# Performance work log

Hardware: AMD Instinct MI355X
Metric: run time of the kernel (lower is better)

## Reference

```python
import jax, jax.numpy as jnp
import numpy as np

P = 20            # corr_patch_size: displacement offsets in [-10, 9]
B, C, H, W = 8, 64, 64, 192


def _leaky(x):
    return jax.nn.leaky_relu(x, 0.1)


def _conv3d(x, w, b, stride, pad, groups):
    y = jax.lax.conv_general_dilated(
        x, w, window_strides=(stride, stride, stride),
        padding=[(pad, pad)] * 3,
        dimension_numbers=('NCDHW', 'OIDHW', 'NCDHW'),
        feature_group_count=groups)
    return y + b[None, :, None, None, None]


def _block(x, dw_w, dw_b, pw_w, pw_b, stride):
    # depthwise 3x3x3 (strided) -> LeakyReLU -> pointwise 1x1x1 -> LeakyReLU
    x = _leaky(_conv3d(x, dw_w, dw_b, stride, 1, x.shape[1]))
    x = _leaky(_conv3d(x, pw_w, pw_b, 1, 0, 1))
    return x


def _correlation(rgb, depth):
    # SpatialCorrelationSampler(kernel_size=1, patch_size=P, stride=1):
    # corr[b, di, dj, y, x] = sum_c rgb[b,c,y,x] * depth[b,c, y+di-P//2, x+dj-P//2]
    pad_lo, pad_hi = P // 2, P - 1 - P // 2   # offsets -10 .. 9
    dp = jnp.pad(depth, ((0, 0), (0, 0), (pad_lo, pad_hi), (pad_lo, pad_hi)))
    rows = []
    for di in range(P):                       # structural loop over patch rows
        dh = dp[:, :, di:di + H, :]           # [B, C, H, W+P-1]
        # all P horizontal shifts at once: [B, P, C, H, W]
        win = jnp.stack([dh[:, :, :, dj:dj + W] for dj in range(P)], axis=1)
        rows.append(jnp.einsum('bchw,bpchw->bphw', rgb, win))
    return jnp.stack(rows, axis=1)            # [B, P, P, H, W]


def setup_inputs() -> dict:
    key = jax.random.key(0)
    ks = jax.random.split(key, 12)

    def rn(k, shape, scale=0.05):
        return jax.random.normal(k, shape, jnp.float32) * scale

    return {
        'rgb_branch': jax.random.normal(ks[0], (B, C, H, W), jnp.float32),
        'depth_branch': jax.random.normal(ks[1], (B, C, H, W), jnp.float32),
        'dw1_w': rn(ks[2], (20, 1, 3, 3, 3)), 'dw1_b': jnp.zeros((20,), jnp.float32),
        'pw1_w': rn(ks[3], (20, 20, 1, 1, 1)), 'pw1_b': jnp.zeros((20,), jnp.float32),
        'dw2_w': rn(ks[4], (20, 1, 3, 3, 3)), 'dw2_b': jnp.zeros((20,), jnp.float32),
        'pw2_w': rn(ks[5], (40, 20, 1, 1, 1)), 'pw2_b': jnp.zeros((40,), jnp.float32),
        'dw3_w': rn(ks[6], (40, 1, 3, 3, 3)), 'dw3_b': jnp.zeros((40,), jnp.float32),
        'pw3_w': rn(ks[7], (40, 40, 1, 1, 1)), 'pw3_b': jnp.zeros((40,), jnp.float32),
        'dw4_w': rn(ks[8], (40, 1, 3, 3, 3)), 'dw4_b': jnp.zeros((40,), jnp.float32),
        'pw4_w': rn(ks[9], (80, 40, 1, 1, 1)), 'pw4_b': jnp.zeros((80,), jnp.float32),
    }


def reference(rgb_branch, depth_branch,
              dw1_w, dw1_b, pw1_w, pw1_b,
              dw2_w, dw2_b, pw2_w, pw2_b,
              dw3_w, dw3_b, pw3_w, pw3_b,
              dw4_w, dw4_b, pw4_w, pw4_b):
    corr = _correlation(rgb_branch, depth_branch)          # [B,20,20,H,W]
    out = _block(corr, dw1_w, dw1_b, pw1_w, pw1_b, 1)      # [B,20,20,H,W]
    out = _block(out, dw2_w, dw2_b, pw2_w, pw2_b, 2)       # [B,40,10,H/2,W/2]
    out = _block(out, dw3_w, dw3_b, pw3_w, pw3_b, 1)
    out = _block(out, dw4_w, dw4_b, pw4_w, pw4_b, 2)       # [B,80,5,H/4,W/4]
    return out
```

## Files before the change

### kernel.cpp

```cpp
#include <hip/hip_runtime.h>
#include <cstdint>
#include <cstddef>


typedef unsigned short u16;
typedef _Float16 f16_t;
typedef __attribute__((ext_vector_type(2))) _Float16 half2_t;
typedef __attribute__((ext_vector_type(8))) _Float16 half8_t;
typedef __attribute__((ext_vector_type(4))) float f32x4;

static __device__ inline u16 f2h(float f) {
    union { f16_t h; u16 u; } v; v.h = (f16_t)f; return v.u;
}
static __device__ inline half2_t H2(uint32_t u) {
    union { uint32_t u; half2_t h; } v; v.u = u; return v.h;
}

#if __has_builtin(__builtin_amdgcn_fdot2)
static __device__ inline float FDOT2(half2_t a, half2_t b, float c) {
    return __builtin_amdgcn_fdot2(a, b, c, false);
}
#else
static __device__ inline float FDOT2(half2_t a, half2_t b, float c) {
    return fmaf((float)a.x, (float)b.x, fmaf((float)a.y, (float)b.y, c));
}
#endif

#if __has_builtin(__builtin_amdgcn_alignbit)
static __device__ inline uint32_t mkp(uint32_t lo, uint32_t hi) {
    return __builtin_amdgcn_alignbit(hi, lo, 16);
}
#else
static __device__ inline uint32_t mkp(uint32_t lo, uint32_t hi) {
    return (lo >> 16) | (hi << 16);
}
#endif

static __device__ inline uint32_t ldu(const u16* p) { return *(const uint32_t*)p; }

__global__ __launch_bounds__(256) void transpose_f16(
        const float* __restrict__ rgb, const float* __restrict__ dep,
        u16* __restrict__ rgbT, u16* __restrict__ depT) {
    const int bh = blockIdx.x;
    const float* src = blockIdx.y ? dep : rgb;
    u16* dst = blockIdx.y ? depT : rgbT;
    const int tid = threadIdx.x;
    const int b = bh >> 6, h = bh & 63;

    __shared__ u16 S[64 * 194];

    const float* srcb = src + (size_t)b * 786432 + (size_t)h * 192;
#pragma unroll
    for (int it = 0; it < 12; ++it) {
        const int idx = it * 256 + tid;
        const int c = idx / 48, w4 = idx - c * 48;
        const float4 v = *(const float4*)(srcb + (size_t)c * 12288 + 4 * w4);
        u16* sp = &S[c * 194 + 4 * w4];
        sp[0] = f2h(v.x); sp[1] = f2h(v.y); sp[2] = f2h(v.z); sp[3] = f2h(v.w);
    }
    __syncthreads();
    u16* dstb = dst + (size_t)bh * 192 * 64;
#pragma unroll
    for (int it = 0; it < 12; ++it) {
        const int idx = it * 256 + tid;
        const int w = idx >> 4, c4 = idx & 15;
        ushort4 o;
        o.x = S[(4 * c4 + 0) * 194 + w];
        o.y = S[(4 * c4 + 1) * 194 + w];
        o.z = S[(4 * c4 + 2) * 194 + w];
        o.w = S[(4 * c4 + 3) * 194 + w];
        *(ushort4*)(dstb + (size_t)w * 64 + 4 * c4) = o;
    }
}

__global__ __launch_bounds__(256) void corr_mfma(
        const u16* __restrict__ rgbT, const u16* __restrict__ depT,
        u16* __restrict__ out) {
    const int idx = blockIdx.x;
    const int band = idx & 7;
    const int j    = idx >> 3;
    const int dig  = j % 5;
    const int rest = j / 5;
    const int h    = band * 8 + (rest & 7);
    const int b    = rest >> 3;
    const int tid = threadIdx.x;
    const int lane = tid & 63, wave = tid >> 6;
    const int n = lane & 15, q = lane >> 4;
    const int w0base = wave * 48;

    __shared__ u16 D4[4][4080];

    const u16* Abase = rgbT + (size_t)(b * 64 + h) * 12288;
    half8_t a0[3], a1[3];
#pragma unroll
    for (int t = 0; t < 3; ++t) {
        const half8_t* Ap = (const half8_t*)(Abase + (size_t)(w0base + t * 16 + n) * 64 + q * 8);
        a0[t] = Ap[0];
        a1[t] = Ap[4];
    }

#pragma unroll
    for (int i = 0; i < 4; ++i) {
        const int di = dig * 4 + i;
        const int hd = h + di - 10;
        if (hd < 0 || hd >= 64) continue;

        const u16* Bbase = depT + (size_t)(b * 64 + hd) * 12288;
        half8_t B0[5], B1[5];
#pragma unroll
        for (int k = 0; k < 5; ++k) {
            const int u0 = w0base + (k - 1) * 16;
            if (u0 >= 0 && u0 <= 176) {
                const half8_t* Bp = (const half8_t*)(Bbase + (size_t)(u0 + n) * 64 + q * 8);
                B0[k] = Bp[0];
                B1[k] = Bp[4];
            } else {
                B0[k] = (half8_t)(f16_t)0.f;
                B1[k] = (half8_t)(f16_t)0.f;
            }
        }
#pragma unroll
        for (int t = 0; t < 3; ++t) {
            const int w0 = w0base + t * 16;
            f32x4 acc[3];
#pragma unroll
            for (int ut = 0; ut < 3; ++ut) {
                acc[ut].x = 0.f; acc[ut].y = 0.f; acc[ut].z = 0.f; acc[ut].w = 0.f;
            }
#pragma unroll
            for (int ut = 0; ut < 3; ++ut) {
                const int k = t + ut;
                acc[ut] = __builtin_amdgcn_mfma_f32_16x16x32_f16(a0[t], B0[k], acc[ut], 0, 0, 0);
                acc[ut] = __builtin_amdgcn_mfma_f32_16x16x32_f16(a1[t], B1[k], acc[ut], 0, 0, 0);
            }
#pragma unroll
            for (int ut = 0; ut < 3; ++ut) {
#pragma unroll
                for (int r = 0; r < 4; ++r) {
                    const int dj = 16 * ut + n - 4 * q - r - 6;
                    const int w = w0 + 4 * q + r;
                    if (dj >= 0 && dj < 20)
                        D4[i][w * 21 + (w >> 2) + dj] = f2h(acc[ut][r]);
                }
            }
        }
    }

#pragma unroll
    for (int i = 0; i < 4; ++i) {
        const int di = dig * 4 + i;
        const int hd = h + di - 10;
        const bool valid = (hd >= 0) && (hd < 64);
        u16* outb = out + ((size_t)((b * 20 + di) * 20) * 64 + h) * 192;
#pragma unroll
        for (int it = 0; it < 4; ++it) {
            const int item = it * 64 + lane;
            if (item < 240) {
                const int dj = item / 12;
                const int w4 = wave * 12 + (item - dj * 12);
                ushort4 o;
                if (valid) {
                    const int base = 85 * w4 + dj;
                    o.x = D4[i][base];
                    o.y = D4[i][base + 21];
                    o.z = D4[i][base + 42];
                    o.w = D4[i][base + 63];
                } else {
                    o = make_ushort4(0, 0, 0, 0);
                }
                *(ushort4*)(outb + (size_t)dj * 12288 + 4 * w4) = o;
            }
        }
    }
}

template<int CIN, int COUT, int S, int DT, int DIN, int HIN, int WIN,
         int DO, int HO, int WO, typename TOUT>
static __device__ __forceinline__ void fused_impl(
        const u16* __restrict__ x,
        const float* __restrict__ dw_w, const float* __restrict__ dw_b,
        const float* __restrict__ pw_w, const float* __restrict__ pw_b,
        TOUT* __restrict__ y) {
    static_assert(WO % 48 == 0 && HO % 4 == 0, "tile divisibility");
    constexpr int CINP = (CIN == 20) ? 22 : 42;
    constexpr int NTASK = CIN * 12;
    constexpr int WT = WO / 48;
    constexpr int NP = S * (DT - 1) + 3;
    constexpr int ROWS = 3 * S + 3;
    constexpr int NL = (S == 1) ? 4 : 5;
    constexpr int G  = (S == 1) ? 6 : 3;
    constexpr int NG = ROWS / G;

    const int wt = blockIdx.x % WT;
    const int ht = blockIdx.x / WT;
    const int d0 = blockIdx.y * DT;
    const int b  = blockIdx.z;
    const int tid = threadIdx.x;
    const int h0 = ht * 4;
    const int wbase = wt * 48;

    __shared__ float sDW[CIN * 27];
    __shared__ float sDB[CIN];
    __shared__ u16   sT[DT * 4 * 48 * CINP + 16];

    for (int i = tid; i < CIN * 27; i += 256) sDW[i] = dw_w[i];
    for (int i = tid; i < CIN; i += 256) sDB[i] = dw_b[i];
    __syncthreads();

    for (int idx = tid; idx < NTASK; idx += 256) {
        const int ci = idx / 12;
        const int wg = idx - ci * 12;
        const int w0g = wbase + wg * 4;
        const int offA = (w0g > 0) ? -2 : 0;

        half2_t KA[9], KB[9];
#pragma unroll
        for (int t = 0; t < 9; ++t) {
            const int kd = t / 3, kh = t - 3 * kd;
            const float k0 = sDW[ci * 27 + kd * 9 + kh * 3 + 0];
            const float k1 = sDW[ci * 27 + kd * 9 + kh * 3 + 1];
            const float k2 = sDW[ci * 27 + kd * 9 + kh * 3 + 2];
            half2_t a; a.x = (f16_t)k0; a.y = (f16_t)k1; KA[t] = a;
            half2_t bb;
            if constexpr (S == 1) { bb.x = (f16_t)k2; bb.y = (f16_t)0.f; }
            else                  { bb.x = (f16_t)0.f; bb.y = (f16_t)k2; }
            KB[t] = bb;
        }

        float acc[DT][4][4];
#pragma unroll
        for (int dl = 0; dl < DT; ++dl)
#pragma unroll
            for (int a = 0; a < 4; ++a)
#pragma unroll
                for (int c = 0; c < 4; ++c) acc[dl][a][c] = 0.f;

        const u16* plane0 = x + (size_t)(b * CIN + ci) * DIN * HIN * WIN;
#pragma unroll
        for (int p = 0; p < NP; ++p) {
            const int din = S * d0 - 1 + p;
            if (din < 0 || din >= DIN) continue;
            const u16* pl = plane0 + (size_t)din * HIN * WIN;
#pragma unroll
            for (int g = 0; g < NG; ++g) {
                uint32_t R[G][NL];
#pragma unroll
                for (int rr = 0; rr < G; ++rr) {
                    const int r = g * G + rr;
                    int hin = h0 * S - 1 + r;
                    int hc = hin < 0 ? 0 : (hin >= HIN ? HIN - 1 : hin);
                    const u16* rowp = pl + (size_t)hc * WIN + (size_t)w0g * S;
                    R[rr][0] = ldu(rowp + offA);
                    R[rr][1] = ldu(rowp);
                    R[rr][2] = ldu(rowp + 2);
                    R[rr][3] = ldu(rowp + 4);
                    if constexpr (S == 2) R[rr][4] = ldu(rowp + 6);
                }
#pragma unroll
                for (int rr = 0; rr < G; ++rr) {
                    const int r = g * G + rr;
                    const int hin = h0 * S - 1 + r;
                    uint32_t D0 = R[rr][0], D1 = R[rr][1];
                    uint32_t D2 = R[rr][2], D3 = R[rr][3];
                    uint32_t E4 = 0;
                    if constexpr (S == 2) E4 = R[rr][4];
                    D0 = (w0g > 0) ? D0 : 0u;
                    if constexpr (S == 1) D3 = (w0g + 4 < WIN) ? D3 : 0u;
                    if constexpr (S == 1) {
                        if (r == 0 || r == ROWS - 1) {
                            const bool rv = (hin >= 0) && (hin < HIN);
                            if (!rv) { D0 = 0; D1 = 0; D2 = 0; D3 = 0; }
                        }
                    } else {
                        if (r == 0) {
                            const bool rv = (hin >= 0);
                            if (!rv) { D0 = 0; D1 = 0; D2 = 0; D3 = 0; E4 = 0; }
                        }
                    }
                    uint32_t PA[4], PB[4];
                    if constexpr (S == 1) {
                        const uint32_t m01 = mkp(D0, D1);
                        const uint32_t m12 = mkp(D1, D2);
                        const uint32_t m23 = mkp(D2, D3);
                        PA[0] = m01; PA[1] = D1; PA[2] = m12; PA[3] = D2;
                        PB[0] = m12; PB[1] = D2; PB[2] = m23; PB[3] = D3;
                    } else {
                        PA[0] = mkp(D0, D1); PA[1] = mkp(D1, D2);
                        PA[2] = mkp(D2, D3); PA[3] = mkp(D3, E4);
                        PB[0] = D1; PB[1] = D2; PB[2] = D3; PB[3] = E4;
                    }
#pragma unroll
                    for (int dl = 0; dl < DT; ++dl) {
                        const int kd = p - S * dl;
                        if (kd < 0 || kd > 2) continue;
#pragma unroll
                        for (int hh = 0; hh < 4; ++hh) {
                            const int kh = r - S * hh;
                            if (kh < 0 || kh > 2) continue;
                            const int t = kd * 3 + kh;
#pragma unroll
                            for (int k = 0; k < 4; ++k)
                                acc[dl][hh][k] = FDOT2(H2(PB[k]), KB[t],
                                                 FDOT2(H2(PA[k]), KA[t],
                                                       acc[dl][hh][k]));
                        }
                    }
                }
            }
        }

        const float bia = sDB[ci];
#pragma unroll
        for (int dl = 0; dl < DT; ++dl) {
#pragma unroll
            for (int hh = 0; hh < 4; ++hh) {
#pragma unroll
                for (int k = 0; k < 4; ++k) {
                    const float t = acc[dl][hh][k] + bia;
                    sT[((dl * 4 + hh) * 48 + wg * 4 + k) * CINP + ci] =
                        f2h(fmaxf(t, 0.1f * t));
                }
            }
        }
    }
    __syncthreads();

    constexpr int NT = (COUT + 15) / 16;
    constexpr int KH = (CIN + 31) / 32;
    constexpr int MTW = DT * 3;
    const int lane = tid & 63, wave = tid >> 6;
    const int m15 = lane & 15, q = lane >> 4;

    half8_t bf[NT][KH];
    float   pb[NT];
#pragma unroll
    for (int nt = 0; nt < NT; ++nt) {
        const int co = nt * 16 + m15;
        pb[nt] = (co < COUT) ? pw_b[co] : 0.f;
#pragma unroll
        for (int kh = 0; kh < KH; ++kh) {
            union { half8_t v; f16_t e[8]; } u;
#pragma unroll
            for (int j = 0; j < 8; ++j) {
                const int ci = kh * 32 + q * 8 + j;
                u.e[j] = (co < COUT && ci < CIN)
                         ? (f16_t)pw_w[co * CIN + ci] : (f16_t)0.f;
            }
            bf[nt][kh] = u.v;
        }
    }

    const size_t planeSz = (size_t)DO * HO * WO;
    for (int mt = wave * MTW; mt < (wave + 1) * MTW; ++mt) {
        const int dl  = mt / 12;
        const int rem = mt - dl * 12;
        const int hh  = rem / 3;
        const int w0  = (rem - hh * 3) * 16;
        if (d0 + dl >= DO) continue;

        const int pos0 = (dl * 4 + hh) * 48 + w0 + m15;
        const u16* ap = &sT[(size_t)pos0 * CINP];
        union { uint32_t u[4]; half8_t v; } af[KH];
#pragma unroll
        for (int kh = 0; kh < KH; ++kh) {
            const int ci0 = kh * 32 + q * 8;
            af[kh].u[0] = (ci0     < CIN) ? ldu(ap + ci0)     : 0u;
            af[kh].u[1] = (ci0 + 2 < CIN) ? ldu(ap + ci0 + 2) : 0u;
            af[kh].u[2] = (ci0 + 4 < CIN) ? ldu(ap + ci0 + 4) : 0u;
            af[kh].u[3] = (ci0 + 6 < CIN) ? ldu(ap + ci0 + 6) : 0u;
        }
#pragma unroll
        for (int nt = 0; nt < NT; ++nt) {
            f32x4 acc;
            acc.x = 0.f; acc.y = 0.f; acc.z = 0.f; acc.w = 0.f;
#pragma unroll
            for (int kh = 0; kh < KH; ++kh)
                acc = __builtin_amdgcn_mfma_f32_16x16x32_f16(
                          af[kh].v, bf[nt][kh], acc, 0, 0, 0);
            const int co = nt * 16 + m15;
            if (co < COUT) {
                const float bias = pb[nt];
                TOUT* yp = y + (size_t)b * COUT * planeSz + (size_t)co * planeSz
                             + (size_t)(d0 + dl) * HO * WO
                             + (size_t)(h0 + hh) * WO + wbase + w0 + q * 4;
                float s0 = acc.x + bias, s1 = acc.y + bias;
                float s2 = acc.z + bias, s3 = acc.w + bias;
                s0 = fmaxf(s0, 0.1f * s0); s1 = fmaxf(s1, 0.1f * s1);
                s2 = fmaxf(s2, 0.1f * s2); s3 = fmaxf(s3, 0.1f * s3);
                if constexpr (sizeof(TOUT) == 4) {
                    float4 o; o.x = s0; o.y = s1; o.z = s2; o.w = s3;
                    *(float4*)yp = o;
                } else {
                    ushort4 o;
                    o.x = f2h(s0); o.y = f2h(s1); o.z = f2h(s2); o.w = f2h(s3);
                    *(ushort4*)yp = o;
                }
            }
        }
    }
}

__global__ __launch_bounds__(256) void fb1_dwpw(
        const u16* __restrict__ x, const float* __restrict__ dww,
        const float* __restrict__ dwb, const float* __restrict__ pww,
        const float* __restrict__ pwb, u16* __restrict__ y) {
    fused_impl<20, 20, 1, 2, 20, 64, 192, 20, 64, 192, u16>(x, dww, dwb, pww, pwb, y);
}
__global__ __launch_bounds__(256) void fb2_dwpw(
        const u16* __restrict__ x, const float* __restrict__ dww,
        const float* __restrict__ dwb, const float* __restrict__ pww,
        const float* __restrict__ pwb, u16* __restrict__ y) {
    fused_impl<20, 40, 2, 2, 20, 64, 192, 10, 32, 96, u16>(x, dww, dwb, pww, pwb, y);
}
__global__ __launch_bounds__(256) void fb3_dwpw(
        const u16* __restrict__ x, const float* __restrict__ dww,
        const float* __restrict__ dwb, const float* __restrict__ pww,
        const float* __restrict__ pwb, u16* __restrict__ y) {
    fused_impl<40, 40, 1, 1, 10, 32, 96, 10, 32, 96, u16>(x, dww, dwb, pww, pwb, y);
}
__global__ __launch_bounds__(256) void fb4_dwpw(
        const u16* __restrict__ x, const float* __restrict__ dww,
        const float* __restrict__ dwb, const float* __restrict__ pww,
        const float* __restrict__ pwb, float* __restrict__ y) {
    fused_impl<40, 80, 2, 1, 10, 32, 96, 5, 16, 48, float>(x, dww, dwb, pww, pwb, y);
}

extern "C" void kernel_launch(void* const* d_in, const int* in_sizes, int n_in,
                              void* d_out, int out_size, void* d_ws, size_t ws_size,
                              hipStream_t stream) {
    const float* rgb  = (const float*)d_in[0];
    const float* dep  = (const float*)d_in[1];
    const float* dw1w = (const float*)d_in[2];
    const float* dw1b = (const float*)d_in[3];
    const float* pw1w = (const float*)d_in[4];
    const float* pw1b = (const float*)d_in[5];
    const float* dw2w = (const float*)d_in[6];
    const float* dw2b = (const float*)d_in[7];
    const float* pw2w = (const float*)d_in[8];
    const float* pw2b = (const float*)d_in[9];
    const float* dw3w = (const float*)d_in[10];
    const float* dw3b = (const float*)d_in[11];
    const float* pw3w = (const float*)d_in[12];
    const float* pw3b = (const float*)d_in[13];
    const float* dw4w = (const float*)d_in[14];
    const float* dw4b = (const float*)d_in[15];
    const float* pw4w = (const float*)d_in[16];
    const float* pw4b = (const float*)d_in[17];

    const size_t HALF = 78643200;
    u16* corrO = (u16*)d_ws;
    u16* rgbT  = (u16*)((char*)d_ws + HALF);
    u16* depT  = (u16*)((char*)d_ws + HALF + 12582912);
    u16* b1o   = (u16*)((char*)d_ws + HALF);
    u16* b2o   = (u16*)d_ws;
    u16* b3o   = (u16*)((char*)d_ws + HALF);
    float* outp = (float*)d_out;

    transpose_f16<<<dim3(512, 2), 256, 0, stream>>>(rgb, dep, rgbT, depT);

    corr_mfma<<<dim3(2560), 256, 0, stream>>>(rgbT, depT, corrO);

    fb1_dwpw<<<dim3(64, 10, 8), 256, 0, stream>>>(corrO, dw1w, dw1b, pw1w, pw1b, b1o);
    fb2_dwpw<<<dim3(16, 5, 8), 256, 0, stream>>>(b1o, dw2w, dw2b, pw2w, pw2b, b2o);
    fb3_dwpw<<<dim3(16, 10, 8), 256, 0, stream>>>(b2o, dw3w, dw3b, pw3w, pw3b, b3o);
    fb4_dwpw<<<dim3(4, 5, 8), 256, 0, stream>>>(b3o, dw4w, dw4b, pw4w, pw4b, outp);
}
```

Before: 353.1 us.

## Double-buffer depthwise input row loads and hoist pointwise weight gather

Restructures the depthwise loop into flattened batches over (depth plane, row group) and uses two register buffers, so the global loads for the next batch are issued before computing the current one. Out-of-range depth planes are now clamped and loaded, then skipped at compute time. Pointwise weight gathering moves before the first barrier when it is small, or into the gap before the second barrier otherwise, to overlap its global latency. All four kernels also get launch_bounds min-blocks of 4, which caps registers per thread and may cause spills given the larger live register set.

```diff
diff --git a/kernel.cpp b/kernel.cpp
--- a/kernel.cpp
+++ b/kernel.cpp
@@ -190,6 +190,9 @@
     constexpr int NL = (S == 1) ? 4 : 5;
     constexpr int G  = (S == 1) ? 6 : 3;
     constexpr int NG = ROWS / G;
+    constexpr int NB = NP * NG;
+    constexpr int NT = (COUT + 15) / 16;
+    constexpr int KH = (CIN + 31) / 32;
 
     const int wt = blockIdx.x % WT;
     const int ht = blockIdx.x / WT;
@@ -205,6 +208,31 @@
 
     for (int i = tid; i < CIN * 27; i += 256) sDW[i] = dw_w[i];
     for (int i = tid; i < CIN; i += 256) sDB[i] = dw_b[i];
+
+    const int lane = tid & 63, wave = tid >> 6;
+    const int m15 = lane & 15, q = lane >> 4;
+
+    half8_t bf[NT][KH];
+    float   pb[NT];
+    auto gather_w = [&]() {
+#pragma unroll
+        for (int nt = 0; nt < NT; ++nt) {
+            const int co = nt * 16 + m15;
+            pb[nt] = (co < COUT) ? pw_b[co] : 0.f;
+#pragma unroll
+            for (int kh = 0; kh < KH; ++kh) {
+                union { half8_t v; f16_t e[8]; } u;
+#pragma unroll
+                for (int jj = 0; jj < 8; ++jj) {
+                    const int ci = kh * 32 + q * 8 + jj;
+                    u.e[jj] = (co < COUT && ci < CIN)
+                              ? (f16_t)pw_w[co * CIN + ci] : (f16_t)0.f;
+                }
+                bf[nt][kh] = u.v;
+            }
+        }
+    };
+    if constexpr (NT * KH <= 4) gather_w();
     __syncthreads();
 
     for (int idx = tid; idx < NTASK; idx += 256) {
@@ -236,77 +264,91 @@
                 for (int c = 0; c < 4; ++c) acc[dl][a][c] = 0.f;
 
         const u16* plane0 = x + (size_t)(b * CIN + ci) * DIN * HIN * WIN;
-#pragma unroll
-        for (int p = 0; p < NP; ++p) {
+
+        uint32_t Rb[2][G * NL];
+
+        auto load_batch = [&](int bi, uint32_t* R) {
+            const int p = bi / NG;
+            const int g = bi - p * NG;
+            int din = S * d0 - 1 + p;
+            int dc = din < 0 ? 0 : (din >= DIN ? DIN - 1 : din);
+            const u16* pl = plane0 + (size_t)dc * HIN * WIN;
+#pragma unroll
+            for (int rr = 0; rr < G; ++rr) {
+                const int r = g * G + rr;
+                int hin = h0 * S - 1 + r;
+                int hc = hin < 0 ? 0 : (hin >= HIN ? HIN - 1 : hin);
+                const u16* rowp = pl + (size_t)hc * WIN + (size_t)w0g * S;
+                R[rr * NL + 0] = ldu(rowp + offA);
+                R[rr * NL + 1] = ldu(rowp);
+                R[rr * NL + 2] = ldu(rowp + 2);
+                R[rr * NL + 3] = ldu(rowp + 4);
+                if constexpr (S == 2) R[rr * NL + 4] = ldu(rowp + 6);
+            }
+        };
+
+        auto compute_batch = [&](int bi, const uint32_t* R) {
+            const int p = bi / NG;
+            const int g = bi - p * NG;
             const int din = S * d0 - 1 + p;
-            if (din < 0 || din >= DIN) continue;
-            const u16* pl = plane0 + (size_t)din * HIN * WIN;
-#pragma unroll
-            for (int g = 0; g < NG; ++g) {
-                uint32_t R[G][NL];
-#pragma unroll
-                for (int rr = 0; rr < G; ++rr) {
-                    const int r = g * G + rr;
-                    int hin = h0 * S - 1 + r;
-                    int hc = hin < 0 ? 0 : (hin >= HIN ? HIN - 1 : hin);
-                    const u16* rowp = pl + (size_t)hc * WIN + (size_t)w0g * S;
-                    R[rr][0] = ldu(rowp + offA);
-                    R[rr][1] = ldu(rowp);
-                    R[rr][2] = ldu(rowp + 2);
-                    R[rr][3] = ldu(rowp + 4);
-                    if constexpr (S == 2) R[rr][4] = ldu(rowp + 6);
-                }
-#pragma unroll
-                for (int rr = 0; rr < G; ++rr) {
-                    const int r = g * G + rr;
-                    const int hin = h0 * S - 1 + r;
-                    uint32_t D0 = R[rr][0], D1 = R[rr][1];
-                    uint32_t D2 = R[rr][2], D3 = R[rr][3];
-                    uint32_t E4 = 0;
-                    if constexpr (S == 2) E4 = R[rr][4];
-                    D0 = (w0g > 0) ? D0 : 0u;
-                    if constexpr (S == 1) D3 = (w0g + 4 < WIN) ? D3 : 0u;
-                    if constexpr (S == 1) {
-                        if (r == 0 || r == ROWS - 1) {
-                            const bool rv = (hin >= 0) && (hin < HIN);
-                            if (!rv) { D0 = 0; D1 = 0; D2 = 0; D3 = 0; }
-                        }
-                    } else {
-                        if (r == 0) {
-                            const bool rv = (hin >= 0);
-                            if (!rv) { D0 = 0; D1 = 0; D2 = 0; D3 = 0; E4 = 0; }
-                        }
+            if (din < 0 || din >= DIN) return;
+#pragma unroll
+            for (int rr = 0; rr < G; ++rr) {
+                const int r = g * G + rr;
+                const int hin = h0 * S - 1 + r;
+                uint32_t D0 = R[rr * NL + 0], D1 = R[rr * NL + 1];
+                uint32_t D2 = R[rr * NL + 2], D3 = R[rr * NL + 3];
+                uint32_t E4 = 0;
+                if constexpr (S == 2) E4 = R[rr * NL + 4];
+                D0 = (w0g > 0) ? D0 : 0u;
+                if constexpr (S == 1) D3 = (w0g + 4 < WIN) ? D3 : 0u;
+                if constexpr (S == 1) {
+                    if (r == 0 || r == ROWS - 1) {
+                        const bool rv = (hin >= 0) && (hin < HIN);
+                        if (!rv) { D0 = 0; D1 = 0; D2 = 0; D3 = 0; }
                     }
-                    uint32_t PA[4], PB[4];
-                    if constexpr (S == 1) {
-                        const uint32_t m01 = mkp(D0, D1);
-                        const uint32_t m12 = mkp(D1, D2);
-                        const uint32_t m23 = mkp(D2, D3);
-                        PA[0] = m01; PA[1] = D1; PA[2] = m12; PA[3] = D2;
-                        PB[0] = m12; PB[1] = D2; PB[2] = m23; PB[3] = D3;
-                    } else {
-                        PA[0] = mkp(D0, D1); PA[1] = mkp(D1, D2);
-                        PA[2] = mkp(D2, D3); PA[3] = mkp(D3, E4);
-                        PB[0] = D1; PB[1] = D2; PB[2] = D3; PB[3] = E4;
+                } else {
+                    if (r == 0) {
+                        const bool rv = (hin >= 0);
+                        if (!rv) { D0 = 0; D1 = 0; D2 = 0; D3 = 0; E4 = 0; }
                     }
-#pragma unroll
-                    for (int dl = 0; dl < DT; ++dl) {
-                        const int kd = p - S * dl;
-                        if (kd < 0 || kd > 2) continue;
-#pragma unroll
-                        for (int hh = 0; hh < 4; ++hh) {
-                            const int kh = r - S * hh;
-                            if (kh < 0 || kh > 2) continue;
-                            const int t = kd * 3 + kh;
-#pragma unroll
-                            for (int k = 0; k < 4; ++k)
-                                acc[dl][hh][k] = FDOT2(H2(PB[k]), KB[t],
-                                                 FDOT2(H2(PA[k]), KA[t],
-                                                       acc[dl][hh][k]));
-                        }
+                }
+                uint32_t PA[4], PB[4];
+                if constexpr (S == 1) {
+                    const uint32_t m01 = mkp(D0, D1);
+                    const uint32_t m12 = mkp(D1, D2);
+                    const uint32_t m23 = mkp(D2, D3);
+                    PA[0] = m01; PA[1] = D1; PA[2] = m12; PA[3] = D2;
+                    PB[0] = m12; PB[1] = D2; PB[2] = m23; PB[3] = D3;
+                } else {
+                    PA[0] = mkp(D0, D1); PA[1] = mkp(D1, D2);
+                    PA[2] = mkp(D2, D3); PA[3] = mkp(D3, E4);
+                    PB[0] = D1; PB[1] = D2; PB[2] = D3; PB[3] = E4;
+                }
+#pragma unroll
+                for (int dl = 0; dl < DT; ++dl) {
+                    const int kd = p - S * dl;
+                    if (kd < 0 || kd > 2) continue;
+#pragma unroll
+                    for (int hh = 0; hh < 4; ++hh) {
+                        const int kh = r - S * hh;
+                        if (kh < 0 || kh > 2) continue;
+                        const int t = kd * 3 + kh;
+#pragma unroll
+                        for (int k = 0; k < 4; ++k)
+                            acc[dl][hh][k] = FDOT2(H2(PB[k]), KB[t],
+                                             FDOT2(H2(PA[k]), KA[t],
+                                                   acc[dl][hh][k]));
                     }
                 }
             }
+        };
+
+        load_batch(0, Rb[0]);
+#pragma unroll
+        for (int bi = 0; bi < NB; ++bi) {
+            if (bi + 1 < NB) load_batch(bi + 1, Rb[(bi + 1) & 1]);
+            compute_batch(bi, Rb[bi & 1]);
         }
 
         const float bia = sDB[ci];
@@ -323,33 +365,10 @@
             }
         }
     }
+    if constexpr (NT * KH > 4) gather_w();
     __syncthreads();
 
-    constexpr int NT = (COUT + 15) / 16;
-    constexpr int KH = (CIN + 31) / 32;
     constexpr int MTW = DT * 3;
-    const int lane = tid & 63, wave = tid >> 6;
-    const int m15 = lane & 15, q = lane >> 4;
-
-    half8_t bf[NT][KH];
-    float   pb[NT];
-#pragma unroll
-    for (int nt = 0; nt < NT; ++nt) {
-        const int co = nt * 16 + m15;
-        pb[nt] = (co < COUT) ? pw_b[co] : 0.f;
-#pragma unroll
-        for (int kh = 0; kh < KH; ++kh) {
-            union { half8_t v; f16_t e[8]; } u;
-#pragma unroll
-            for (int j = 0; j < 8; ++j) {
-                const int ci = kh * 32 + q * 8 + j;
-                u.e[j] = (co < COUT && ci < CIN)
-                         ? (f16_t)pw_w[co * CIN + ci] : (f16_t)0.f;
-            }
-            bf[nt][kh] = u.v;
-        }
-    }
-
     const size_t planeSz = (size_t)DO * HO * WO;
     for (int mt = wave * MTW; mt < (wave + 1) * MTW; ++mt) {
         const int dl  = mt / 12;
@@ -400,25 +419,25 @@
     }
 }
 
-__global__ __launch_bounds__(256) void fb1_dwpw(
+__global__ __launch_bounds__(256, 4) void fb1_dwpw(
         const u16* __restrict__ x, const float* __restrict__ dww,
         const float* __restrict__ dwb, const float* __restrict__ pww,
         const float* __restrict__ pwb, u16* __restrict__ y) {
     fused_impl<20, 20, 1, 2, 20, 64, 192, 20, 64, 192, u16>(x, dww, dwb, pww, pwb, y);
 }
-__global__ __launch_bounds__(256) void fb2_dwpw(
+__global__ __launch_bounds__(256, 4) void fb2_dwpw(
         const u16* __restrict__ x, const float* __restrict__ dww,
         const float* __restrict__ dwb, const float* __restrict__ pww,
         const float* __restrict__ pwb, u16* __restrict__ y) {
     fused_impl<20, 40, 2, 2, 20, 64, 192, 10, 32, 96, u16>(x, dww, dwb, pww, pwb, y);
 }
-__global__ __launch_bounds__(256) void fb3_dwpw(
+__global__ __launch_bounds__(256, 4) void fb3_dwpw(
         const u16* __restrict__ x, const float* __restrict__ dww,
         const float* __restrict__ dwb, const float* __restrict__ pww,
         const float* __restrict__ pwb, u16* __restrict__ y) {
     fused_impl<40, 40, 1, 1, 10, 32, 96, 10, 32, 96, u16>(x, dww, dwb, pww, pwb, y);
 }
-__global__ __launch_bounds__(256) void fb4_dwpw(
+__global__ __launch_bounds__(256, 4) void fb4_dwpw(
         const u16* __restrict__ x, const float* __restrict__ dww,
         const float* __restrict__ dwb, const float* __restrict__ pww,
         const float* __restrict__ pwb, float* __restrict__ y) {
```

Result: slower. 375.0 us (+6.2%).
